# Kernel tuning notes

Measured on AMD Instinct MI355X. Metric: run time of the kernel, lower is better.

Reference implementation:

```python
import jax, jax.numpy as jnp
import numpy as np

NUM_HEADS = 8
EPS = 1e-12  # torch F.normalize eps


def _l2norm(t):
    n = jnp.linalg.norm(t, axis=-1, keepdims=True)
    return t / jnp.maximum(n, EPS)


def setup_inputs() -> dict:
    key = jax.random.key(0)
    k1, k2, k3 = jax.random.split(key, 3)
    B, T, N, D = 16, 12, 1024, 128
    x = jax.random.normal(k1, (B, T, N, D), dtype=jnp.float32)
    # Linear(model_dim, 3*model_dim, bias=False): stored as (D, 3D) for x @ W
    W_qkv = jax.random.normal(k2, (D, 3 * D), dtype=jnp.float32) * (1.0 / np.sqrt(D))
    W_out = jax.random.normal(k3, (D, D), dtype=jnp.float32) * (1.0 / np.sqrt(D))
    b_out = jnp.zeros((D,), dtype=jnp.float32)
    return {"x": x, "W_qkv": W_qkv, "W_out": W_out, "b_out": b_out}


def reference(x, W_qkv, W_out, b_out):
    B, T, N, D = x.shape
    H = NUM_HEADS
    hd = D // H
    qkv = x @ W_qkv                                  # (B,T,N,3D)
    q, k, v = jnp.split(qkv, 3, axis=-1)
    # split heads + flatten (B,T) -> b = B*T, matching torch stack/flatten
    qs = _l2norm(q.reshape(B * T, N, H, hd))          # (b,N,H,m)
    ks = _l2norm(k.reshape(B * T, N, H, hd))
    vs = v.reshape(B * T, N, H, hd)
    # linear attention: running kv sum + normalizer
    kvs = jnp.einsum('blhm,blhd->bhmd', ks, vs)       # (b,H,m,d)
    attn_num = jnp.einsum('bnhm,bhmd->bnhd', qs, kvs) + N * vs
    ks_sum = jnp.sum(ks, axis=1)                      # (b,H,m)
    normalizer = jnp.einsum('bnhm,bhm->bnh', qs, ks_sum)[..., None] + N
    out = attn_num / normalizer                       # (b,N,H,d)
    out = out.reshape(B, T, N, D)
    return out @ W_out + b_out
```

## Files before the change

### kernel.cpp

```cpp
#include <hip/hip_runtime.h>

#define NBATCH 192
#define SEQ    1024
#define DIM    128
#define NH     8
#define EPS    1e-12f

typedef short bf16x8 __attribute__((ext_vector_type(8)));
typedef float f32x4  __attribute__((ext_vector_type(4)));

#define KVS_F  393216
#define ZERO_F 417792

static __device__ __forceinline__ unsigned short f2bf(float f) {
    unsigned u = __builtin_bit_cast(unsigned, f);
    u += 0x7fff + ((u >> 16) & 1);
    return (unsigned short)(u >> 16);
}

template <int CTRL>
static __device__ __forceinline__ float dpp_add(float v) {
    int j = __builtin_amdgcn_mov_dpp(__builtin_bit_cast(int, v), CTRL, 0xf, 0xf, false);
    return v + __builtin_bit_cast(float, j);
}
static __device__ __forceinline__ float r16sum(float v) {
    v = dpp_add<0xB1>(v);
    v = dpp_add<0x4E>(v);
    v = dpp_add<0x141>(v);
    v = dpp_add<0x140>(v);
    return v;
}

static __device__ __forceinline__ int strip_addr(int row, int el) {
    return row * 32 + ((((el >> 3) ^ (row & 3)) << 3) | (el & 7));
}

static __device__ __forceinline__ void stage_w(unsigned short* lds,
                                               const unsigned short* __restrict__ gT, int t) {
#pragma unroll
    for (int i = 0; i < 4; ++i) {
        int idx = i * 512 + t, n = idx >> 4, gr = idx & 15;
        uint4 v = *reinterpret_cast<const uint4*>(gT + n * 128 + gr * 8);
        *reinterpret_cast<uint4*>(lds + n * 128 + ((gr ^ (n & 15)) << 3)) = v;
    }
}

static __device__ __forceinline__ bf16x8 wfrag(const unsigned short* lds, int ct, int ks,
                                               int q, int n15) {
    return *reinterpret_cast<const bf16x8*>(
        lds + (ct * 16 + n15) * 128 + ((((ks << 2) + q) ^ n15) << 3));
}

static __device__ __forceinline__ uint2 pack4(float a, float b, float c, float d) {
    uint2 r;
    r.x = (unsigned)f2bf(a) | ((unsigned)f2bf(b) << 16);
    r.y = (unsigned)f2bf(c) | ((unsigned)f2bf(d) << 16);
    return r;
}

static __device__ __forceinline__ bf16x8 cvt8(float4 a, float4 b) {
    bf16x8 r;
    r[0] = (short)f2bf(a.x); r[1] = (short)f2bf(a.y); r[2] = (short)f2bf(a.z); r[3] = (short)f2bf(a.w);
    r[4] = (short)f2bf(b.x); r[5] = (short)f2bf(b.y); r[6] = (short)f2bf(b.z); r[7] = (short)f2bf(b.w);
    return r;
}

__global__ __launch_bounds__(256) void k0_prep(const float* __restrict__ Wqkv,
                                               const float* __restrict__ Wout,
                                               float* __restrict__ zero_p,
                                               unsigned short* __restrict__ wsWT) {
    int bid = blockIdx.x, t = threadIdx.x;
    if (bid < 1632) { zero_p[bid * 256 + t] = 0.0f; return; }
    int i = (bid - 1632) * 256 + t;
    int which = i >> 14, e = i & 16383;
    int n = e & 127, c = e >> 7;
    float v = (which < 3) ? Wqkv[c * 384 + which * 128 + n] : Wout[c * 128 + n];
    wsWT[which * 16384 + n * 128 + c] = f2bf(v);
}

__global__ __launch_bounds__(512, 4) void k1_kv(const float* __restrict__ x,
                                                const unsigned short* __restrict__ wsWT,
                                                float* __restrict__ kvs_ws,
                                                float* __restrict__ kssum_ws) {
    __shared__ unsigned short lds[40960];
    unsigned short* wk = lds;
    unsigned short* wv = lds + 16384;
    int t = threadIdx.x, w = t >> 6, lane = t & 63, q = lane >> 4, n15 = lane & 15;
    int b = blockIdx.x >> 2, seg = blockIdx.x & 3;

    stage_w(wk, wsWT + 1 * 16384, t);
    stage_w(wv, wsWT + 2 * 16384, t);
    unsigned short* knS = lds + 32768 + w * 1024;
    unsigned short* vS  = knS + 512;

    bf16x8 ah[2][4];
#pragma unroll
    for (int rs = 0; rs < 2; ++rs) {
        int row = seg * 256 + w * 32 + rs * 16 + n15;
        const float* xr = x + (size_t)(b * SEQ + row) * DIM;
#pragma unroll
        for (int ks = 0; ks < 4; ++ks) {
            float4 p0 = *reinterpret_cast<const float4*>(xr + ks * 32 + q * 8);
            float4 p1 = *reinterpret_cast<const float4*>(xr + ks * 32 + q * 8 + 4);
            ah[rs][ks] = cvt8(p0, p1);
        }
    }
    __syncthreads();

    f32x4 kvsacc[8];
    float ksum[8];
#pragma unroll
    for (int h = 0; h < 8; ++h) { kvsacc[h] = (f32x4){0,0,0,0}; ksum[h] = 0.f; }

#pragma unroll
    for (int ct = 0; ct < 8; ++ct) {
        f32x4 ka[2] = {(f32x4){0,0,0,0}, (f32x4){0,0,0,0}};
        f32x4 va[2] = {(f32x4){0,0,0,0}, (f32x4){0,0,0,0}};
#pragma unroll
        for (int ks = 0; ks < 4; ++ks) {
            bf16x8 kb = wfrag(wk, ct, ks, q, n15);
            bf16x8 vb = wfrag(wv, ct, ks, q, n15);
#pragma unroll
            for (int rs = 0; rs < 2; ++rs) {
                ka[rs] = __builtin_amdgcn_mfma_f32_16x16x32_bf16(ah[rs][ks], kb, ka[rs], 0, 0, 0);
                va[rs] = __builtin_amdgcn_mfma_f32_16x16x32_bf16(ah[rs][ks], vb, va[rs], 0, 0, 0);
            }
        }
#pragma unroll
        for (int rs = 0; rs < 2; ++rs) {
            float kn[4];
#pragma unroll
            for (int r = 0; r < 4; ++r) {
                float val = ka[rs][r];
                float ssq = r16sum(val * val);
                float di  = 1.0f / fmaxf(sqrtf(ssq), EPS);
                kn[r] = val * di;
                ksum[ct] += kn[r];
            }
            *reinterpret_cast<uint2*>(knS + strip_addr(n15, rs * 16 + q * 4)) =
                pack4(kn[0], kn[1], kn[2], kn[3]);
            *reinterpret_cast<uint2*>(vS + strip_addr(n15, rs * 16 + q * 4)) =
                pack4(va[rs][0], va[rs][1], va[rs][2], va[rs][3]);
        }
        bf16x8 aK = *reinterpret_cast<const bf16x8*>(knS + strip_addr(n15, q * 8));
        bf16x8 bV = *reinterpret_cast<const bf16x8*>(vS + strip_addr(n15, q * 8));
        kvsacc[ct] = __builtin_amdgcn_mfma_f32_16x16x32_bf16(aK, bV, kvsacc[ct], 0, 0, 0);
    }

#pragma unroll
    for (int ct = 0; ct < 8; ++ct) {
        float s = ksum[ct];
        s += __shfl_xor(s, 16); s += __shfl_xor(s, 32);
        if (lane < 16) atomicAdd(&kssum_ws[b * 128 + ct * 16 + n15], s);
    }

    __syncthreads();
    float* red = reinterpret_cast<float*>(lds);
#pragma unroll
    for (int ct = 0; ct < 8; ++ct)
#pragma unroll
        for (int r = 0; r < 4; ++r)
            red[w * 2048 + ct * 256 + (q * 4 + r) * 16 + n15] = kvsacc[ct][r];
    __syncthreads();
#pragma unroll
    for (int i = 0; i < 4; ++i) {
        int el = i * 512 + t;
        float s = 0.f;
#pragma unroll
        for (int ww = 0; ww < 8; ++ww) s += red[ww * 2048 + el];
        atomicAdd(&kvs_ws[b * 2048 + el], s);
    }
}

__global__ __launch_bounds__(512, 2) void k2_out(const float* __restrict__ x,
                                                 const unsigned short* __restrict__ wsWT,
                                                 const float* __restrict__ kvs_ws,
                                                 const float* __restrict__ kssum_ws,
                                                 const float* __restrict__ bout,
                                                 float* __restrict__ out) {
    __shared__ unsigned short lds[57344];
    unsigned short* wbuf = lds;
    unsigned short* kvsT = lds + 16384;
    unsigned short* qsS  = lds + 20480;
    unsigned short* tile = lds + 24576;
    int t = threadIdx.x, w = t >> 6, lane = t & 63, q = lane >> 4, n15 = lane & 15;
    int b = blockIdx.x >> 2, seg = blockIdx.x & 3, rowbase = seg * 256;

    stage_w(wbuf, wsWT + 2 * 16384, t);
    {
        int row = t >> 2, part = t & 3, h = row >> 4, d = row & 15;
        unsigned es[8];
#pragma unroll
        for (int j = 0; j < 8; j += 2) {
            int m0 = part * 8 + j;
            unsigned lo = (m0     < 16) ? f2bf(kvs_ws[b * 2048 + h * 256 + m0 * 16 + d])      : 0;
            unsigned hi = (m0 + 1 < 16) ? f2bf(kvs_ws[b * 2048 + h * 256 + (m0 + 1) * 16 + d]) : 0;
            es[j] = lo | (hi << 16);
        }
        uint4 v = {es[0], es[2], es[4], es[6]};
        *reinterpret_cast<uint4*>(kvsT + row * 32 + (((part ^ (row & 3)) << 3))) = v;
    }
    {
        unsigned short* s = qsS + w * 512;
        uint2 z = {0, 0};
        *reinterpret_cast<uint2*>(s + strip_addr(n15, 16 + q * 4)) = z;
    }
    float kss[8];
#pragma unroll
    for (int h = 0; h < 8; ++h) kss[h] = kssum_ws[b * 128 + h * 16 + n15];

    bf16x8 ah[2][4];
#pragma unroll
    for (int rs = 0; rs < 2; ++rs) {
        int row = rowbase + w * 32 + rs * 16 + n15;
        const float* xr = x + (size_t)(b * SEQ + row) * DIM;
#pragma unroll
        for (int ks = 0; ks < 4; ++ks) {
            float4 p0 = *reinterpret_cast<const float4*>(xr + ks * 32 + q * 8);
            float4 p1 = *reinterpret_cast<const float4*>(xr + ks * 32 + q * 8 + 4);
            ah[rs][ks] = cvt8(p0, p1);
        }
    }
    __syncthreads();

    f32x4 vacc[2][8];
#pragma unroll
    for (int rs = 0; rs < 2; ++rs)
#pragma unroll
        for (int h = 0; h < 8; ++h) vacc[rs][h] = (f32x4){0,0,0,0};
#pragma unroll
    for (int ct = 0; ct < 8; ++ct)
#pragma unroll
        for (int ks = 0; ks < 4; ++ks) {
            bf16x8 bb = wfrag(wbuf, ct, ks, q, n15);
#pragma unroll
            for (int rs = 0; rs < 2; ++rs)
                vacc[rs][ct] = __builtin_amdgcn_mfma_f32_16x16x32_bf16(ah[rs][ks], bb, vacc[rs][ct], 0, 0, 0);
        }
    __syncthreads();
    stage_w(wbuf, wsWT + 0, t);
    __syncthreads();

    f32x4 qacc[2][8];
#pragma unroll
    for (int rs = 0; rs < 2; ++rs)
#pragma unroll
        for (int h = 0; h < 8; ++h) qacc[rs][h] = (f32x4){0,0,0,0};
#pragma unroll
    for (int ct = 0; ct < 8; ++ct)
#pragma unroll
        for (int ks = 0; ks < 4; ++ks) {
            bf16x8 bb = wfrag(wbuf, ct, ks, q, n15);
#pragma unroll
            for (int rs = 0; rs < 2; ++rs)
                qacc[rs][ct] = __builtin_amdgcn_mfma_f32_16x16x32_bf16(ah[rs][ks], bb, qacc[rs][ct], 0, 0, 0);
        }

    unsigned short* myS = qsS + w * 512;
#pragma unroll
    for (int rs = 0; rs < 2; ++rs)
#pragma unroll
        for (int h = 0; h < 8; ++h) {
            float pv[4];
#pragma unroll
            for (int r = 0; r < 4; ++r) {
                float val = qacc[rs][h][r];
                float ssq = r16sum(val * val);
                float tt  = r16sum(val * kss[h]);
                float di  = 1.0f / fmaxf(sqrtf(ssq), EPS);
                float inv = 1.0f / (tt * di + (float)SEQ);
                pv[r] = val * di * inv;
                vacc[rs][h][r] *= (float)SEQ * inv;
            }
#pragma unroll
            for (int r = 0; r < 4; ++r)
                myS[strip_addr(q * 4 + r, n15)] = f2bf(pv[r]);
            bf16x8 aq = *reinterpret_cast<const bf16x8*>(myS + strip_addr(n15, q * 8));
            bf16x8 bk = *reinterpret_cast<const bf16x8*>(kvsT + strip_addr(h * 16 + n15, q * 8));
            vacc[rs][h] = __builtin_amdgcn_mfma_f32_16x16x32_bf16(aq, bk, vacc[rs][h], 0, 0, 0);
#pragma unroll
            for (int r = 0; r < 4; ++r) {
                int rt = w * 32 + rs * 16 + q * 4 + r;
                int colg = h * 2 + (n15 >> 3);
                tile[rt * 128 + (((colg ^ (rt & 15)) << 3) | (n15 & 7))] = f2bf(vacc[rs][h][r]);
            }
        }

    __syncthreads();
    stage_w(wbuf, wsWT + 3 * 16384, t);
    __syncthreads();

    bf16x8 ap[2][4];
#pragma unroll
    for (int rs = 0; rs < 2; ++rs)
#pragma unroll
        for (int ks = 0; ks < 4; ++ks) {
            int rt = w * 32 + rs * 16 + n15;
            ap[rs][ks] = *reinterpret_cast<const bf16x8*>(
                tile + rt * 128 + ((((ks << 2) + q) ^ (rt & 15)) << 3));
        }
    f32x4 oacc[2][8];
#pragma unroll
    for (int rs = 0; rs < 2; ++rs)
#pragma unroll
        for (int h = 0; h < 8; ++h) oacc[rs][h] = (f32x4){0,0,0,0};
#pragma unroll
    for (int ct = 0; ct < 8; ++ct)
#pragma unroll
        for (int ks = 0; ks < 4; ++ks) {
            bf16x8 bb = wfrag(wbuf, ct, ks, q, n15);
#pragma unroll
            for (int rs = 0; rs < 2; ++rs)
                oacc[rs][ct] = __builtin_amdgcn_mfma_f32_16x16x32_bf16(ap[rs][ks], bb, oacc[rs][ct], 0, 0, 0);
        }
#pragma unroll
    for (int ct = 0; ct < 8; ++ct) {
        float bo = bout[ct * 16 + n15];
#pragma unroll
        for (int rs = 0; rs < 2; ++rs)
#pragma unroll
            for (int r = 0; r < 4; ++r) {
                int row = rowbase + w * 32 + rs * 16 + q * 4 + r;
                out[(size_t)(b * SEQ + row) * DIM + ct * 16 + n15] = oacc[rs][ct][r] + bo;
            }
    }
}

extern "C" void kernel_launch(void* const* d_in, const int* in_sizes, int n_in,
                              void* d_out, int out_size, void* d_ws, size_t ws_size,
                              hipStream_t stream) {
    const float* x    = (const float*)d_in[0];
    const float* Wqkv = (const float*)d_in[1];
    const float* Wout = (const float*)d_in[2];
    const float* bout = (const float*)d_in[3];
    float* out = (float*)d_out;

    float* kvs_ws   = (float*)d_ws;
    float* kssum_ws = kvs_ws + KVS_F;
    unsigned short* wsWT = (unsigned short*)((char*)d_ws + (size_t)ZERO_F * 4);

    k0_prep<<<dim3(1888), dim3(256), 0, stream>>>(Wqkv, Wout, kvs_ws, wsWT);
    k1_kv<<<dim3(768), dim3(512), 0, stream>>>(x, wsWT, kvs_ws, kssum_ws);
    k2_out<<<dim3(768), dim3(512), 0, stream>>>(x, wsWT, kvs_ws, kssum_ws, bout, out);
}
```

Before: 310.0 us.

## Load pre-swizzled MFMA weight fragments from global, drop LDS weight staging

k0_prep now writes the bf16 weights in the exact per-lane MFMA fragment order, so k1 and k2 read B fragments directly from global/L2 instead of staging them into LDS with barriers. k2 is restructured: it computes Q first, folds the normalizer into a per-row scale kept in LDS, and accumulates the V projection into the q·kvs accumulator, which frees registers and LDS and lets occupancy rise to 4 blocks. Workspace zeroing moves to hipMemsetAsync. The cost is more global/L2 traffic for weight fragments, a slight change in rounding order, and an extra memset call.

```diff
diff --git a/kernel.cpp b/kernel.cpp
--- a/kernel.cpp
+++ b/kernel.cpp
@@ -35,22 +35,6 @@
     return row * 32 + ((((el >> 3) ^ (row & 3)) << 3) | (el & 7));
 }
 
-static __device__ __forceinline__ void stage_w(unsigned short* lds,
-                                               const unsigned short* __restrict__ gT, int t) {
-#pragma unroll
-    for (int i = 0; i < 4; ++i) {
-        int idx = i * 512 + t, n = idx >> 4, gr = idx & 15;
-        uint4 v = *reinterpret_cast<const uint4*>(gT + n * 128 + gr * 8);
-        *reinterpret_cast<uint4*>(lds + n * 128 + ((gr ^ (n & 15)) << 3)) = v;
-    }
-}
-
-static __device__ __forceinline__ bf16x8 wfrag(const unsigned short* lds, int ct, int ks,
-                                               int q, int n15) {
-    return *reinterpret_cast<const bf16x8*>(
-        lds + (ct * 16 + n15) * 128 + ((((ks << 2) + q) ^ n15) << 3));
-}
-
 static __device__ __forceinline__ uint2 pack4(float a, float b, float c, float d) {
     uint2 r;
     r.x = (unsigned)f2bf(a) | ((unsigned)f2bf(b) << 16);
@@ -65,32 +49,34 @@
     return r;
 }
 
+static __device__ __forceinline__ bf16x8 gfrag(const unsigned short* __restrict__ wT,
+                                               int ct, int ks, int lane) {
+    return *reinterpret_cast<const bf16x8*>(wT + ((ct * 4 + ks) * 64 + lane) * 8);
+}
+
 __global__ __launch_bounds__(256) void k0_prep(const float* __restrict__ Wqkv,
                                                const float* __restrict__ Wout,
-                                               float* __restrict__ zero_p,
                                                unsigned short* __restrict__ wsWT) {
-    int bid = blockIdx.x, t = threadIdx.x;
-    if (bid < 1632) { zero_p[bid * 256 + t] = 0.0f; return; }
-    int i = (bid - 1632) * 256 + t;
+    int i = blockIdx.x * 256 + threadIdx.x;
     int which = i >> 14, e = i & 16383;
-    int n = e & 127, c = e >> 7;
-    float v = (which < 3) ? Wqkv[c * 384 + which * 128 + n] : Wout[c * 128 + n];
-    wsWT[which * 16384 + n * 128 + c] = f2bf(v);
+    int j = e & 7, f = e >> 3;
+    int n15 = f & 15, q = (f >> 4) & 3, ks = (f >> 6) & 3, ct = f >> 8;
+    int k = ks * 32 + q * 8 + j, n = ct * 16 + n15;
+    float v = (which < 3) ? Wqkv[k * 384 + which * 128 + n] : Wout[k * 128 + n];
+    wsWT[i] = f2bf(v);
 }
 
 __global__ __launch_bounds__(512, 4) void k1_kv(const float* __restrict__ x,
                                                 const unsigned short* __restrict__ wsWT,
                                                 float* __restrict__ kvs_ws,
                                                 float* __restrict__ kssum_ws) {
-    __shared__ unsigned short lds[40960];
-    unsigned short* wk = lds;
-    unsigned short* wv = lds + 16384;
+    __shared__ float redf[16384];
+    unsigned short* strips = reinterpret_cast<unsigned short*>(redf);
     int t = threadIdx.x, w = t >> 6, lane = t & 63, q = lane >> 4, n15 = lane & 15;
     int b = blockIdx.x >> 2, seg = blockIdx.x & 3;
-
-    stage_w(wk, wsWT + 1 * 16384, t);
-    stage_w(wv, wsWT + 2 * 16384, t);
-    unsigned short* knS = lds + 32768 + w * 1024;
+    const unsigned short* wkT = wsWT + 16384;
+    const unsigned short* wvT = wsWT + 32768;
+    unsigned short* knS = strips + w * 1024;
     unsigned short* vS  = knS + 512;
 
     bf16x8 ah[2][4];
@@ -105,7 +91,6 @@
             ah[rs][ks] = cvt8(p0, p1);
         }
     }
-    __syncthreads();
 
     f32x4 kvsacc[8];
     float ksum[8];
@@ -118,8 +103,8 @@
         f32x4 va[2] = {(f32x4){0,0,0,0}, (f32x4){0,0,0,0}};
 #pragma unroll
         for (int ks = 0; ks < 4; ++ks) {
-            bf16x8 kb = wfrag(wk, ct, ks, q, n15);
-            bf16x8 vb = wfrag(wv, ct, ks, q, n15);
+            bf16x8 kb = gfrag(wkT, ct, ks, lane);
+            bf16x8 vb = gfrag(wvT, ct, ks, lane);
 #pragma unroll
             for (int rs = 0; rs < 2; ++rs) {
                 ka[rs] = __builtin_amdgcn_mfma_f32_16x16x32_bf16(ah[rs][ks], kb, ka[rs], 0, 0, 0);
@@ -155,38 +140,38 @@
     }
 
     __syncthreads();
-    float* red = reinterpret_cast<float*>(lds);
 #pragma unroll
     for (int ct = 0; ct < 8; ++ct)
 #pragma unroll
         for (int r = 0; r < 4; ++r)
-            red[w * 2048 + ct * 256 + (q * 4 + r) * 16 + n15] = kvsacc[ct][r];
+            redf[w * 2048 + ct * 256 + (q * 4 + r) * 16 + n15] = kvsacc[ct][r];
     __syncthreads();
 #pragma unroll
     for (int i = 0; i < 4; ++i) {
         int el = i * 512 + t;
         float s = 0.f;
 #pragma unroll
-        for (int ww = 0; ww < 8; ++ww) s += red[ww * 2048 + el];
+        for (int ww = 0; ww < 8; ++ww) s += redf[ww * 2048 + el];
         atomicAdd(&kvs_ws[b * 2048 + el], s);
     }
 }
 
-__global__ __launch_bounds__(512, 2) void k2_out(const float* __restrict__ x,
+__global__ __launch_bounds__(512, 4) void k2_out(const float* __restrict__ x,
                                                  const unsigned short* __restrict__ wsWT,
                                                  const float* __restrict__ kvs_ws,
                                                  const float* __restrict__ kssum_ws,
                                                  const float* __restrict__ bout,
                                                  float* __restrict__ out) {
-    __shared__ unsigned short lds[57344];
-    unsigned short* wbuf = lds;
-    unsigned short* kvsT = lds + 16384;
-    unsigned short* qsS  = lds + 20480;
-    unsigned short* tile = lds + 24576;
+    __shared__ unsigned short lds[40960];
+    unsigned short* kvsT = lds;
+    float* invS = reinterpret_cast<float*>(lds + 4096);
+    unsigned short* tile = lds + 8192;
     int t = threadIdx.x, w = t >> 6, lane = t & 63, q = lane >> 4, n15 = lane & 15;
     int b = blockIdx.x >> 2, seg = blockIdx.x & 3, rowbase = seg * 256;
-
-    stage_w(wbuf, wsWT + 2 * 16384, t);
+    const unsigned short* wqT = wsWT;
+    const unsigned short* wvT = wsWT + 32768;
+    const unsigned short* woT = wsWT + 49152;
+
     {
         int row = t >> 2, part = t & 3, h = row >> 4, d = row & 15;
         unsigned es[8];
@@ -198,13 +183,9 @@
             es[j] = lo | (hi << 16);
         }
         uint4 v = {es[0], es[2], es[4], es[6]};
-        *reinterpret_cast<uint4*>(kvsT + row * 32 + (((part ^ (row & 3)) << 3))) = v;
-    }
-    {
-        unsigned short* s = qsS + w * 512;
-        uint2 z = {0, 0};
-        *reinterpret_cast<uint2*>(s + strip_addr(n15, 16 + q * 4)) = z;
-    }
+        *reinterpret_cast<uint4*>(kvsT + row * 32 + ((part ^ (row & 3)) << 3)) = v;
+    }
+
     float kss[8];
 #pragma unroll
     for (int h = 0; h < 8; ++h) kss[h] = kssum_ws[b * 128 + h * 16 + n15];
@@ -221,42 +202,33 @@
             ah[rs][ks] = cvt8(p0, p1);
         }
     }
+
+    unsigned short* tw   = tile + w * 4096;
+    unsigned short* myS  = tw;
+    float* myInv = invS + w * 256;
+    {
+        uint2 z = {0, 0};
+        *reinterpret_cast<uint2*>(myS + strip_addr(n15, 16 + q * 4)) = z;
+    }
     __syncthreads();
 
-    f32x4 vacc[2][8];
-#pragma unroll
-    for (int rs = 0; rs < 2; ++rs)
-#pragma unroll
-        for (int h = 0; h < 8; ++h) vacc[rs][h] = (f32x4){0,0,0,0};
+    f32x4 qacc[2][8];
+#pragma unroll
+    for (int rs = 0; rs < 2; ++rs)
+#pragma unroll
+        for (int h = 0; h < 8; ++h) qacc[rs][h] = (f32x4){0,0,0,0};
 #pragma unroll
     for (int ct = 0; ct < 8; ++ct)
 #pragma unroll
         for (int ks = 0; ks < 4; ++ks) {
-            bf16x8 bb = wfrag(wbuf, ct, ks, q, n15);
-#pragma unroll
-            for (int rs = 0; rs < 2; ++rs)
-                vacc[rs][ct] = __builtin_amdgcn_mfma_f32_16x16x32_bf16(ah[rs][ks], bb, vacc[rs][ct], 0, 0, 0);
-        }
-    __syncthreads();
-    stage_w(wbuf, wsWT + 0, t);
-    __syncthreads();
-
-    f32x4 qacc[2][8];
-#pragma unroll
-    for (int rs = 0; rs < 2; ++rs)
-#pragma unroll
-        for (int h = 0; h < 8; ++h) qacc[rs][h] = (f32x4){0,0,0,0};
-#pragma unroll
-    for (int ct = 0; ct < 8; ++ct)
-#pragma unroll
-        for (int ks = 0; ks < 4; ++ks) {
-            bf16x8 bb = wfrag(wbuf, ct, ks, q, n15);
+            bf16x8 bb = gfrag(wqT, ct, ks, lane);
 #pragma unroll
             for (int rs = 0; rs < 2; ++rs)
                 qacc[rs][ct] = __builtin_amdgcn_mfma_f32_16x16x32_bf16(ah[rs][ks], bb, qacc[rs][ct], 0, 0, 0);
         }
 
-    unsigned short* myS = qsS + w * 512;
+    const float invSEQ = 1.0f / (float)SEQ;
+    f32x4 nacc[2][8];
 #pragma unroll
     for (int rs = 0; rs < 2; ++rs)
 #pragma unroll
@@ -269,35 +241,48 @@
                 float tt  = r16sum(val * kss[h]);
                 float di  = 1.0f / fmaxf(sqrtf(ssq), EPS);
                 float inv = 1.0f / (tt * di + (float)SEQ);
-                pv[r] = val * di * inv;
-                vacc[rs][h][r] *= (float)SEQ * inv;
+                pv[r] = val * di * invSEQ;
+                if (n15 == 0) myInv[(rs * 16 + q * 4 + r) * 8 + h] = (float)SEQ * inv;
             }
 #pragma unroll
             for (int r = 0; r < 4; ++r)
                 myS[strip_addr(q * 4 + r, n15)] = f2bf(pv[r]);
             bf16x8 aq = *reinterpret_cast<const bf16x8*>(myS + strip_addr(n15, q * 8));
             bf16x8 bk = *reinterpret_cast<const bf16x8*>(kvsT + strip_addr(h * 16 + n15, q * 8));
-            vacc[rs][h] = __builtin_amdgcn_mfma_f32_16x16x32_bf16(aq, bk, vacc[rs][h], 0, 0, 0);
+            nacc[rs][h] = __builtin_amdgcn_mfma_f32_16x16x32_bf16(aq, bk, (f32x4){0,0,0,0}, 0, 0, 0);
+        }
+
+#pragma unroll
+    for (int ct = 0; ct < 8; ++ct)
+#pragma unroll
+        for (int ks = 0; ks < 4; ++ks) {
+            bf16x8 bb = gfrag(wvT, ct, ks, lane);
+#pragma unroll
+            for (int rs = 0; rs < 2; ++rs)
+                nacc[rs][ct] = __builtin_amdgcn_mfma_f32_16x16x32_bf16(ah[rs][ks], bb, nacc[rs][ct], 0, 0, 0);
+        }
+
+#pragma unroll
+    for (int rs = 0; rs < 2; ++rs)
+#pragma unroll
+        for (int h = 0; h < 8; ++h)
 #pragma unroll
             for (int r = 0; r < 4; ++r) {
-                int rt = w * 32 + rs * 16 + q * 4 + r;
+                float invN = myInv[(rs * 16 + q * 4 + r) * 8 + h];
+                float pre  = nacc[rs][h][r] * invN;
+                int rt = rs * 16 + q * 4 + r;
                 int colg = h * 2 + (n15 >> 3);
-                tile[rt * 128 + (((colg ^ (rt & 15)) << 3) | (n15 & 7))] = f2bf(vacc[rs][h][r]);
-            }
-        }
-
-    __syncthreads();
-    stage_w(wbuf, wsWT + 3 * 16384, t);
-    __syncthreads();
+                tw[rt * 128 + (((colg ^ (rt & 15)) << 3) | (n15 & 7))] = f2bf(pre);
+            }
 
     bf16x8 ap[2][4];
 #pragma unroll
     for (int rs = 0; rs < 2; ++rs)
 #pragma unroll
         for (int ks = 0; ks < 4; ++ks) {
-            int rt = w * 32 + rs * 16 + n15;
+            int rt = rs * 16 + n15;
             ap[rs][ks] = *reinterpret_cast<const bf16x8*>(
-                tile + rt * 128 + ((((ks << 2) + q) ^ (rt & 15)) << 3));
+                tw + rt * 128 + ((((ks << 2) + q) ^ (rt & 15)) << 3));
         }
     f32x4 oacc[2][8];
 #pragma unroll
@@ -308,7 +293,7 @@
     for (int ct = 0; ct < 8; ++ct)
 #pragma unroll
         for (int ks = 0; ks < 4; ++ks) {
-            bf16x8 bb = wfrag(wbuf, ct, ks, q, n15);
+            bf16x8 bb = gfrag(woT, ct, ks, lane);
 #pragma unroll
             for (int rs = 0; rs < 2; ++rs)
                 oacc[rs][ct] = __builtin_amdgcn_mfma_f32_16x16x32_bf16(ap[rs][ks], bb, oacc[rs][ct], 0, 0, 0);
@@ -339,7 +324,8 @@
     float* kssum_ws = kvs_ws + KVS_F;
     unsigned short* wsWT = (unsigned short*)((char*)d_ws + (size_t)ZERO_F * 4);
 
-    k0_prep<<<dim3(1888), dim3(256), 0, stream>>>(Wqkv, Wout, kvs_ws, wsWT);
+    hipMemsetAsync(d_ws, 0, (size_t)ZERO_F * 4, stream);
+    k0_prep<<<dim3(256), dim3(256), 0, stream>>>(Wqkv, Wout, wsWT);
     k1_kv<<<dim3(768), dim3(512), 0, stream>>>(x, wsWT, kvs_ws, kssum_ws);
     k2_out<<<dim3(768), dim3(512), 0, stream>>>(x, wsWT, kvs_ws, kssum_ws, bout, out);
 }
```

New measurement: 329.2 us. +6.2%, slower.
